# Optimization experiments

Hardware: AMD Instinct MI355X
Metric: run time of the kernel (lower is better)

## Reference

```python
import jax, jax.numpy as jnp
import numpy as np

B, S, D, H = 2, 4096, 768, 12
HD = D // H  # head_dim = 64


def setup_inputs() -> dict:
    key = jax.random.key(0)
    ks = jax.random.split(key, 12)
    s = 0.02
    inp = {
        'q': jax.random.normal(ks[0], (B, S, D), jnp.float32),
        'k': jax.random.normal(ks[1], (B, S, D), jnp.float32),
        'v': jax.random.normal(ks[2], (B, S, D), jnp.float32),
        # True = masked position (filled with -inf); causal mask, broadcastable
        'mask': jnp.triu(jnp.ones((S, S), jnp.bool_), k=1)[None, None],
        'Wq': jax.random.normal(ks[3], (D, D), jnp.float32) * s,
        'bq': jnp.zeros((D,), jnp.float32),
        'Wk': jax.random.normal(ks[4], (D, D), jnp.float32) * s,
        'bk': jnp.zeros((D,), jnp.float32),
        'Wv': jax.random.normal(ks[5], (D, D), jnp.float32) * s,
        'bv': jnp.zeros((D,), jnp.float32),
        'Wo': jax.random.normal(ks[6], (D, D), jnp.float32) * s,
        'bo': jnp.zeros((D,), jnp.float32),
    }
    return inp


def _split_heads(x):
    # [B, S, D] -> [B, H, S, HD]
    return x.reshape(B, S, H, HD).transpose(0, 2, 1, 3)


def reference(q, k, v, mask, Wq, bq, Wk, bk, Wv, bv, Wo, bo):
    # per-head linear projections (torch Linear: x @ W.T + b)
    qh = _split_heads(q @ Wq.T + bq)
    kh = _split_heads(k @ Wk.T + bk)
    vh = _split_heads(v @ Wv.T + bv)
    scale = 1.0 / np.sqrt(HD).astype(np.float32)
    # naive full [B, H, S, S] attention scores (module materializes these)
    wei = jnp.einsum('bhqd,bhkd->bhqk', qh, kh) * scale
    wei = jnp.where(mask, -jnp.inf, wei)
    attn = jax.nn.softmax(wei, axis=-1)
    feats = jnp.einsum('bhqk,bhkd->bhqd', attn, vh)
    # concat heads: [B, H, S, HD] -> [B, S, D]
    out = feats.transpose(0, 2, 1, 3).reshape(B, S, D)
    return out @ Wo.T + bo
```

## Files before the change

kernel.cpp:

```cpp
#include <hip/hip_runtime.h>
#include <math.h>

#define B_  2
#define S_  4096
#define D_  768
#define H_  12
#define HD_ 64

using bf16x8  = __attribute__((ext_vector_type(8))) __bf16;
using f32x4   = __attribute__((ext_vector_type(4))) float;
using ushort8 = __attribute__((ext_vector_type(8))) unsigned short;
using uintv2  = __attribute__((ext_vector_type(2))) unsigned;
using uintv4  = __attribute__((ext_vector_type(4))) unsigned;

__device__ __forceinline__ unsigned short f2b(float f) {
    union { float f; unsigned u; } x; x.f = f;
    unsigned r = x.u + 0x7fffu + ((x.u >> 16) & 1u);
    return (unsigned short)(r >> 16);
}
__device__ __forceinline__ unsigned pk2(float x, float y) {
    unsigned ux = __builtin_bit_cast(unsigned, x) + 0x8000u;
    unsigned uy = __builtin_bit_cast(unsigned, y) + 0x8000u;
    return (uy & 0xFFFF0000u) | (ux >> 16);
}
__device__ __forceinline__ unsigned cvtpk(float lo, float hi) {
    unsigned r;
    asm("v_cvt_pk_bf16_f32 %0, %1, %2" : "=v"(r) : "v"(lo), "v"(hi));
    return r;
}
__device__ __forceinline__ uintv2 xpose_pair(unsigned x, unsigned y) {
    uintv2 s = __builtin_amdgcn_permlane32_swap(x, y, false, false);
    return __builtin_amdgcn_permlane16_swap(s[0], s[1], false, false);
}

__global__ __launch_bounds__(256)
void w_convert(const float* __restrict__ Wq, const float* __restrict__ Wk,
               const float* __restrict__ Wv, const float* __restrict__ Wo,
               unsigned short* __restrict__ Wb)
{
    const int z = blockIdx.y;
    const float* src = (z == 0) ? Wq : (z == 1) ? Wk : (z == 2) ? Wv : Wo;
    unsigned short* dst = Wb + (size_t)z * (D_ * D_);
    int idx = blockIdx.x * 256 + threadIdx.x;
    const float4 a = *(const float4*)(src + (size_t)idx * 8);
    const float4 b = *(const float4*)(src + (size_t)idx * 8 + 4);
    uint4 o;
    o.x = pk2(a.x, a.y); o.y = pk2(a.z, a.w);
    o.z = pk2(b.x, b.y); o.w = pk2(b.z, b.w);
    *(uint4*)(dst + (size_t)idx * 8) = o;
}

__global__ __launch_bounds__(256)
void qkv_gemm(const float* __restrict__ q, const float* __restrict__ k,
              const float* __restrict__ v,
              const unsigned short* __restrict__ Wb,
              const float* __restrict__ bq, const float* __restrict__ bk,
              const float* __restrict__ bv,
              unsigned short* __restrict__ Qp, unsigned short* __restrict__ Kp,
              unsigned short* __restrict__ Vrm)
{
    constexpr int BM = 128, BN = 128, BK = 32, LDP = 40, NK = D_ / BK;
    const int lin = blockIdx.x;
    const int xcd = lin & 7, s = lin >> 3;
    const int z  = s / 48, rr = s % 48;
    const int bn = rr >> 3;
    const int bm = xcd * 8 + (rr & 7);

    const float* A    = (z == 0) ? q  : (z == 1) ? k  : v;
    const unsigned short* W = Wb + (size_t)z * (D_ * D_);
    const float* bias = (z == 0) ? bq : (z == 1) ? bk : bv;
    unsigned short* C = (z == 0) ? Qp : (z == 1) ? Kp : Vrm;

    __shared__ __align__(16) unsigned short As[2][BM * LDP];
    __shared__ __align__(16) unsigned short Bs[2][BN * LDP];

    const int tid = threadIdx.x;
    const int w = tid >> 6, lane = tid & 63, lr = lane & 15, lg = lane >> 4;
    const int wm = (w >> 1) * 64, wn = (w & 1) * 64;

    const int arow = tid >> 3, ac4 = (tid & 7) * 4;
    const int brow = tid >> 2, bc8 = (tid & 3) * 8;
    const float* Abase = A + (size_t)(bm * BM + arow) * D_ + ac4;
    const unsigned short* Wbase = W + (size_t)(bn * BN + brow) * D_ + bc8;

    float4 ap[4]; ushort8 bp[2];

    for (int t = 0; t < 4; ++t) ap[t] = *(const float4*)(Abase + (size_t)t * 32 * D_);
    for (int t = 0; t < 2; ++t) bp[t] = *(const ushort8*)(Wbase + (size_t)t * 64 * D_);
    for (int t = 0; t < 4; ++t)
        *(uint2*)&As[0][(arow + t * 32) * LDP + ac4] =
            make_uint2(pk2(ap[t].x, ap[t].y), pk2(ap[t].z, ap[t].w));
    for (int t = 0; t < 2; ++t)
        *(ushort8*)&Bs[0][(brow + t * 64) * LDP + bc8] = bp[t];
    __syncthreads();

    f32x4 acc[4][4] = {};

    for (int it = 0; it < NK; ++it) {
        const int cur = it & 1;
        const int k2 = ((it + 1 < NK) ? it + 1 : it) * BK;
        for (int t = 0; t < 4; ++t) ap[t] = *(const float4*)(Abase + k2 + (size_t)t * 32 * D_);
        for (int t = 0; t < 2; ++t) bp[t] = *(const ushort8*)(Wbase + k2 + (size_t)t * 64 * D_);

        bf16x8 af[4], bfr[4];
        for (int i = 0; i < 4; ++i) af[i]  = *(const bf16x8*)&As[cur][(wm + i * 16 + lr) * LDP + lg * 8];
        for (int j = 0; j < 4; ++j) bfr[j] = *(const bf16x8*)&Bs[cur][(wn + j * 16 + lr) * LDP + lg * 8];
        for (int i = 0; i < 4; ++i)
            for (int j = 0; j < 4; ++j)
                acc[i][j] = __builtin_amdgcn_mfma_f32_16x16x32_bf16(af[i], bfr[j], acc[i][j], 0, 0, 0);

        const int nxt = cur ^ 1;
        for (int t = 0; t < 4; ++t)
            *(uint2*)&As[nxt][(arow + t * 32) * LDP + ac4] =
                make_uint2(pk2(ap[t].x, ap[t].y), pk2(ap[t].z, ap[t].w));
        for (int t = 0; t < 2; ++t)
            *(ushort8*)&Bs[nxt][(brow + t * 64) * LDP + bc8] = bp[t];
        __syncthreads();
    }

    const float qscale = 0.18033688011112042f;
    for (int i = 0; i < 4; ++i) {
        int row0 = bm * BM + wm + i * 16 + lg * 4;
        for (int j = 0; j < 4; ++j) {
            int col = bn * BN + wn + j * 16 + lr;
            float bv_ = bias[col];
            for (int r = 0; r < 4; ++r) {
                float val = acc[i][j][r] + bv_;
                if (z == 0) val *= qscale;
                C[(size_t)(row0 + r) * D_ + col] = f2b(val);
            }
        }
    }
}

__global__ __launch_bounds__(256)
void v_transpose(const unsigned short* __restrict__ Vrm,
                 unsigned short* __restrict__ Vt)
{
    __shared__ __align__(16) unsigned short T[64][72];
    const int st = blockIdx.x, bh = blockIdx.y;
    const int b = bh / H_, h = bh % H_;
    const int tid = threadIdx.x;

    for (int t = 0; t < 2; ++t) {
        int idx = tid + t * 256, s = idx >> 3, c8 = (idx & 7) * 8;
        *(ushort8*)&T[s][c8] =
            *(const ushort8*)(Vrm + ((size_t)(b * S_ + st * 64 + s)) * D_ + h * HD_ + c8);
    }
    __syncthreads();
    const int d = tid >> 2;
    for (int it = 0; it < 2; ++it) {
        int s8 = (tid & 3) + it * 4;
        ushort8 val;
        for (int j = 0; j < 8; ++j) val[j] = T[s8 * 8 + j][d];
        *(ushort8*)(Vt + ((size_t)bh * HD_ + d) * S_ + st * 64 + s8 * 8) = val;
    }
}

__global__ __launch_bounds__(256)
void o_gemm(const unsigned short* __restrict__ Ai, const unsigned short* __restrict__ W,
            const float* __restrict__ bias, float* __restrict__ C)
{
    constexpr int BM = 128, BN = 64, BK = 32, LDP = 40, NK = D_ / BK;
    __shared__ __align__(16) unsigned short As[2][BM * LDP];
    __shared__ __align__(16) unsigned short Bs[2][BN * LDP];

    const int lin = blockIdx.x;
    const int xcd = lin & 7, s = lin >> 3;
    const int bn = s >> 3;
    const int bm = xcd * 8 + (s & 7);

    const int tid = threadIdx.x;
    const int w = tid >> 6, lane = tid & 63, lr = lane & 15, lg = lane >> 4;
    const int wm = (w >> 1) * 64, wn = (w & 1) * 32;

    const int arow = tid >> 2, ac8 = (tid & 3) * 8;
    const unsigned short* Abase = Ai + (size_t)(bm * BM + arow) * D_ + ac8;
    const unsigned short* Wbase = W + (size_t)(bn * BN + arow) * D_ + ac8;

    ushort8 apre[2], bpre;
    for (int t = 0; t < 2; ++t) apre[t] = *(const ushort8*)(Abase + (size_t)t * 64 * D_);
    bpre = *(const ushort8*)(Wbase);
    for (int t = 0; t < 2; ++t)
        *(ushort8*)&As[0][(arow + t * 64) * LDP + ac8] = apre[t];
    *(ushort8*)&Bs[0][arow * LDP + ac8] = bpre;
    __syncthreads();

    f32x4 acc[4][2] = {};

    for (int it = 0; it < NK; ++it) {
        const int cur = it & 1;
        const int k2 = ((it + 1 < NK) ? it + 1 : it) * BK;
        for (int t = 0; t < 2; ++t) apre[t] = *(const ushort8*)(Abase + k2 + (size_t)t * 64 * D_);
        bpre = *(const ushort8*)(Wbase + k2);

        bf16x8 af[4], bfr[2];
        for (int i = 0; i < 4; ++i) af[i]  = *(const bf16x8*)&As[cur][(wm + i * 16 + lr) * LDP + lg * 8];
        for (int j = 0; j < 2; ++j) bfr[j] = *(const bf16x8*)&Bs[cur][(wn + j * 16 + lr) * LDP + lg * 8];
        for (int i = 0; i < 4; ++i)
            for (int j = 0; j < 2; ++j)
                acc[i][j] = __builtin_amdgcn_mfma_f32_16x16x32_bf16(af[i], bfr[j], acc[i][j], 0, 0, 0);

        const int nxt = cur ^ 1;
        for (int t = 0; t < 2; ++t)
            *(ushort8*)&As[nxt][(arow + t * 64) * LDP + ac8] = apre[t];
        *(ushort8*)&Bs[nxt][arow * LDP + ac8] = bpre;
        __syncthreads();
    }

    for (int i = 0; i < 4; ++i) {
        int row0 = bm * BM + wm + i * 16 + lg * 4;
        for (int j = 0; j < 2; ++j) {
            int col = bn * BN + wn + j * 16 + lr;
            float bv_ = bias[col];
            for (int r = 0; r < 4; ++r)
                C[(size_t)(row0 + r) * D_ + col] = acc[i][j][r] + bv_;
        }
    }
}

__global__ __launch_bounds__(256)
void attn_kernel(const unsigned short* __restrict__ Qp,
                 const unsigned short* __restrict__ Kp,
                 const unsigned short* __restrict__ Vt,
                 unsigned short* __restrict__ feats)
{
    __shared__ __align__(16) unsigned short Ks[2][64 * 72];
    __shared__ __align__(16) unsigned short Vs[2][64 * 72];

    const int tid = threadIdx.x;
    const int lin = blockIdx.x + gridDim.x * blockIdx.y;
    const int xcd = lin & 7, idx = lin >> 3;
    const int bhl = idx >> 5;
    const int i   = idx & 31;
    int p;
    if (bhl == 0)      p = i;
    else if (bhl == 1) p = (i + 16) & 31;
    else               p = (i < 16) ? (31 - 2 * i) : (62 - 2 * i);
    const int bh  = xcd * 3 + bhl;
    const int b = bh / H_, h = bh % H_;
    const int w = tid >> 6, lane = tid & 63, lr = lane & 15, lg = lane >> 4;

    const int qtA = 63 - p, qtB = p;

    bf16x8 ones;
    for (int j = 0; j < 8; ++j) ones[j] = (__bf16)1.0f;

    const size_t kbase = ((size_t)b * S_) * D_ + h * HD_;
    const size_t vbase = ((size_t)bh * HD_) * S_;

    const size_t qbA = ((size_t)(b * S_ + qtA * 64 + w * 16 + lr)) * D_ + h * HD_;
    const size_t qbB = ((size_t)(b * S_ + qtB * 64 + w * 16 + lr)) * D_ + h * HD_;
    bf16x8 qfA0 = *(const bf16x8*)(Qp + qbA + lg * 8);
    bf16x8 qfA1 = *(const bf16x8*)(Qp + qbA + 32 + lg * 8);
    bf16x8 qfB0 = *(const bf16x8*)(Qp + qbB + lg * 8);
    bf16x8 qfB1 = *(const bf16x8*)(Qp + qbB + 32 + lg * 8);

    f32x4 oA[4] = {}, oB[4] = {};
    f32x4 lA = {0.f, 0.f, 0.f, 0.f}, lB = {0.f, 0.f, 0.f, 0.f};

    const int nst = qtA + 1;

    const int srow = tid >> 3, sc8 = (tid & 7) * 8;
    const unsigned short* kpt = Kp + kbase + (size_t)srow * D_ + sc8;
    const unsigned short* vpt = Vt + vbase + (size_t)srow * S_ + sc8;
    unsigned short* KsW0 = &Ks[0][srow * 72 + sc8];
    unsigned short* VsW0 = &Vs[0][srow * 72 + sc8];
    unsigned short* KsW1 = &Ks[1][srow * 72 + sc8];
    unsigned short* VsW1 = &Vs[1][srow * 72 + sc8];

    {
        ushort8 a0 = *(const ushort8*)(kpt);
        ushort8 a1 = *(const ushort8*)(kpt + (size_t)32 * D_);
        ushort8 a2 = *(const ushort8*)(vpt);
        ushort8 a3 = *(const ushort8*)(vpt + (size_t)32 * S_);
        *(ushort8*)KsW0            = a0;
        *(ushort8*)(KsW0 + 32*72)  = a1;
        *(ushort8*)VsW0            = a2;
        *(ushort8*)(VsW0 + 32*72)  = a3;
    }
    __syncthreads();

    for (int kb = 0; kb < nst; ++kb) {
        const bool bAct = (kb <= qtB);
        const int cur = kb & 1;
        const unsigned short* Kc = Ks[cur];
        const unsigned short* Vc = Vs[cur];

        const int kb2 = (kb + 1 < nst) ? kb + 1 : kb;
        const unsigned short* kp2 = kpt + (size_t)kb2 * 64 * D_;
        const unsigned short* vp2 = vpt + (size_t)kb2 * 64;
        ushort8 kr0 = *(const ushort8*)(kp2);
        ushort8 kr1 = *(const ushort8*)(kp2 + (size_t)32 * D_);
        ushort8 vr0 = *(const ushort8*)(vp2);
        ushort8 vr1 = *(const ushort8*)(vp2 + (size_t)32 * S_);

        bf16x8 kf[4][2];
        for (int n = 0; n < 4; ++n) {
            kf[n][0] = *(const bf16x8*)&Kc[(n * 16 + lr) * 72 + lg * 8];
            kf[n][1] = *(const bf16x8*)&Kc[(n * 16 + lr) * 72 + 32 + lg * 8];
        }

        bf16x8 pfA0, pfA1, pfB0, pfB1;

        {
            f32x4 st[4];
            for (int n = 0; n < 4; ++n) {
                f32x4 s = {0.f, 0.f, 0.f, 0.f};
                s = __builtin_amdgcn_mfma_f32_16x16x32_bf16(kf[n][0], qfA0, s, 0, 0, 0);
                s = __builtin_amdgcn_mfma_f32_16x16x32_bf16(kf[n][1], qfA1, s, 0, 0, 0);
                st[n] = s;
            }
            if (kb == qtA) {
                for (int n = 0; n < 4; ++n)
                    for (int r = 0; r < 4; ++r)
                        if (n * 16 + lg * 4 + r > w * 16 + lr) st[n][r] = -INFINITY;
            }
            unsigned a_[4][2];
            for (int n = 0; n < 4; ++n) {
                float e0 = __builtin_amdgcn_exp2f(st[n][0]);
                float e1 = __builtin_amdgcn_exp2f(st[n][1]);
                float e2 = __builtin_amdgcn_exp2f(st[n][2]);
                float e3 = __builtin_amdgcn_exp2f(st[n][3]);
                a_[n][0] = cvtpk(e0, e1);
                a_[n][1] = cvtpk(e2, e3);
            }
            uintv2 p00 = xpose_pair(a_[0][0], a_[1][0]);
            uintv2 p01 = xpose_pair(a_[0][1], a_[1][1]);
            uintv2 p10 = xpose_pair(a_[2][0], a_[3][0]);
            uintv2 p11 = xpose_pair(a_[2][1], a_[3][1]);
            uintv4 w0 = {p00[0], p01[0], p00[1], p01[1]};
            uintv4 w1 = {p10[0], p11[0], p10[1], p11[1]};
            pfA0 = __builtin_bit_cast(bf16x8, w0);
            pfA1 = __builtin_bit_cast(bf16x8, w1);
        }
        if (bAct) {
            f32x4 st[4];
            for (int n = 0; n < 4; ++n) {
                f32x4 s = {0.f, 0.f, 0.f, 0.f};
                s = __builtin_amdgcn_mfma_f32_16x16x32_bf16(kf[n][0], qfB0, s, 0, 0, 0);
                s = __builtin_amdgcn_mfma_f32_16x16x32_bf16(kf[n][1], qfB1, s, 0, 0, 0);
                st[n] = s;
            }
            if (kb == qtB) {
                for (int n = 0; n < 4; ++n)
                    for (int r = 0; r < 4; ++r)
                        if (n * 16 + lg * 4 + r > w * 16 + lr) st[n][r] = -INFINITY;
            }
            unsigned a_[4][2];
            for (int n = 0; n < 4; ++n) {
                float e0 = __builtin_amdgcn_exp2f(st[n][0]);
                float e1 = __builtin_amdgcn_exp2f(st[n][1]);
                float e2 = __builtin_amdgcn_exp2f(st[n][2]);
                float e3 = __builtin_amdgcn_exp2f(st[n][3]);
                a_[n][0] = cvtpk(e0, e1);
                a_[n][1] = cvtpk(e2, e3);
            }
            uintv2 p00 = xpose_pair(a_[0][0], a_[1][0]);
            uintv2 p01 = xpose_pair(a_[0][1], a_[1][1]);
            uintv2 p10 = xpose_pair(a_[2][0], a_[3][0]);
            uintv2 p11 = xpose_pair(a_[2][1], a_[3][1]);
            uintv4 w0 = {p00[0], p01[0], p00[1], p01[1]};
            uintv4 w1 = {p10[0], p11[0], p10[1], p11[1]};
            pfB0 = __builtin_bit_cast(bf16x8, w0);
            pfB1 = __builtin_bit_cast(bf16x8, w1);
        }

        bf16x8 vf[4][2];
        for (int n = 0; n < 4; ++n) {
            vf[n][0] = *(const bf16x8*)&Vc[(n * 16 + lr) * 72 + lg * 8];
            vf[n][1] = *(const bf16x8*)&Vc[(n * 16 + lr) * 72 + 32 + lg * 8];
        }
        {
            for (int n = 0; n < 4; ++n) {
                oA[n] = __builtin_amdgcn_mfma_f32_16x16x32_bf16(vf[n][0], pfA0, oA[n], 0, 0, 0);
                oA[n] = __builtin_amdgcn_mfma_f32_16x16x32_bf16(vf[n][1], pfA1, oA[n], 0, 0, 0);
            }
            lA = __builtin_amdgcn_mfma_f32_16x16x32_bf16(ones, pfA0, lA, 0, 0, 0);
            lA = __builtin_amdgcn_mfma_f32_16x16x32_bf16(ones, pfA1, lA, 0, 0, 0);
        }
        if (bAct) {
            for (int n = 0; n < 4; ++n) {
                oB[n] = __builtin_amdgcn_mfma_f32_16x16x32_bf16(vf[n][0], pfB0, oB[n], 0, 0, 0);
                oB[n] = __builtin_amdgcn_mfma_f32_16x16x32_bf16(vf[n][1], pfB1, oB[n], 0, 0, 0);
            }
            lB = __builtin_amdgcn_mfma_f32_16x16x32_bf16(ones, pfB0, lB, 0, 0, 0);
            lB = __builtin_amdgcn_mfma_f32_16x16x32_bf16(ones, pfB1, lB, 0, 0, 0);
        }

        if (cur == 0) {
            *(ushort8*)KsW1            = kr0;
            *(ushort8*)(KsW1 + 32*72)  = kr1;
            *(ushort8*)VsW1            = vr0;
            *(ushort8*)(VsW1 + 32*72)  = vr1;
        } else {
            *(ushort8*)KsW0            = kr0;
            *(ushort8*)(KsW0 + 32*72)  = kr1;
            *(ushort8*)VsW0            = vr0;
            *(ushort8*)(VsW0 + 32*72)  = vr1;
        }
        __syncthreads();
    }

    {
        const float inv = 1.0f / lA[0];
        const size_t obase = ((size_t)(b * S_ + qtA * 64 + w * 16 + lr)) * D_ + h * HD_;
        for (int n = 0; n < 4; ++n) {
            unsigned short e0 = f2b(oA[n][0] * inv), e1 = f2b(oA[n][1] * inv);
            unsigned short e2 = f2b(oA[n][2] * inv), e3 = f2b(oA[n][3] * inv);
            *(uint2*)(feats + obase + n * 16 + lg * 4) =
                make_uint2((unsigned)e0 | ((unsigned)e1 << 16),
                           (unsigned)e2 | ((unsigned)e3 << 16));
        }
    }
    {
        const float inv = 1.0f / lB[0];
        const size_t obase = ((size_t)(b * S_ + qtB * 64 + w * 16 + lr)) * D_ + h * HD_;
        for (int n = 0; n < 4; ++n) {
            unsigned short e0 = f2b(oB[n][0] * inv), e1 = f2b(oB[n][1] * inv);
            unsigned short e2 = f2b(oB[n][2] * inv), e3 = f2b(oB[n][3] * inv);
            *(uint2*)(feats + obase + n * 16 + lg * 4) =
                make_uint2((unsigned)e0 | ((unsigned)e1 << 16),
                           (unsigned)e2 | ((unsigned)e3 << 16));
        }
    }
}

extern "C" void kernel_launch(void* const* d_in, const int* in_sizes, int n_in,
                              void* d_out, int out_size, void* d_ws, size_t ws_size,
                              hipStream_t stream) {
    const float* q  = (const float*)d_in[0];
    const float* k  = (const float*)d_in[1];
    const float* v  = (const float*)d_in[2];
    const float* Wq = (const float*)d_in[4];
    const float* bq = (const float*)d_in[5];
    const float* Wk = (const float*)d_in[6];
    const float* bk = (const float*)d_in[7];
    const float* Wv = (const float*)d_in[8];
    const float* bv = (const float*)d_in[9];
    const float* Wo = (const float*)d_in[10];
    const float* bo = (const float*)d_in[11];
    float* out = (float*)d_out;

    const size_t npro = (size_t)B_ * S_ * D_;
    const size_t nw   = (size_t)D_ * D_;
    unsigned short* Qp    = (unsigned short*)d_ws;
    unsigned short* Kp    = Qp + npro;
    unsigned short* Vrm   = Kp + npro;
    unsigned short* Vt    = Vrm + npro;
    unsigned short* Wb    = Vt + npro;
    unsigned short* feats = Vrm;

    dim3 blk(256);
    w_convert<<<dim3(288, 4), blk, 0, stream>>>(Wq, Wk, Wv, Wo, Wb);
    qkv_gemm<<<dim3(1152), blk, 0, stream>>>(q, k, v, Wb, bq, bk, bv,
                                             Qp, Kp, Vrm);
    v_transpose<<<dim3(S_ / 64, B_ * H_), blk, 0, stream>>>(Vrm, Vt);
    attn_kernel<<<dim3(32, B_ * H_), blk, 0, stream>>>(Qp, Kp, Vt, feats);
    o_gemm<<<dim3(768), blk, 0, stream>>>(feats, Wb + 3 * nw, bo, out);
}
```

Measured before the change: 327.3 us.

## Fuse V transpose into QKV GEMM epilogue and raise MFMA wave priority

The QKV projection epilogue now writes V directly in the head-major transposed layout the attention kernel consumes, so the separate v_transpose kernel and its intermediate buffer go away. This saves one launch plus a full read and write of V. The transposed stores are 8-byte scattered writes and less coalesced than before. Separately, the attention kernel raises wave priority around its MFMA blocks to help the scheduler overlap matrix work with other waves.

```diff
diff --git a/kernel.cpp b/kernel.cpp
--- a/kernel.cpp
+++ b/kernel.cpp
@@ -57,7 +57,7 @@
               const float* __restrict__ bq, const float* __restrict__ bk,
               const float* __restrict__ bv,
               unsigned short* __restrict__ Qp, unsigned short* __restrict__ Kp,
-              unsigned short* __restrict__ Vrm)
+              unsigned short* __restrict__ Vt)
 {
     constexpr int BM = 128, BN = 128, BK = 32, LDP = 40, NK = D_ / BK;
     const int lin = blockIdx.x;
@@ -69,7 +69,6 @@
     const float* A    = (z == 0) ? q  : (z == 1) ? k  : v;
     const unsigned short* W = Wb + (size_t)z * (D_ * D_);
     const float* bias = (z == 0) ? bq : (z == 1) ? bk : bv;
-    unsigned short* C = (z == 0) ? Qp : (z == 1) ? Kp : Vrm;
 
     __shared__ __align__(16) unsigned short As[2][BM * LDP];
     __shared__ __align__(16) unsigned short Bs[2][BN * LDP];
@@ -118,42 +117,38 @@
         __syncthreads();
     }
 
-    const float qscale = 0.18033688011112042f;
-    for (int i = 0; i < 4; ++i) {
-        int row0 = bm * BM + wm + i * 16 + lg * 4;
+    if (z == 2) {
         for (int j = 0; j < 4; ++j) {
-            int col = bn * BN + wn + j * 16 + lr;
-            float bv_ = bias[col];
-            for (int r = 0; r < 4; ++r) {
-                float val = acc[i][j][r] + bv_;
-                if (z == 0) val *= qscale;
-                C[(size_t)(row0 + r) * D_ + col] = f2b(val);
-            }
-        }
-    }
-}
-
-__global__ __launch_bounds__(256)
-void v_transpose(const unsigned short* __restrict__ Vrm,
-                 unsigned short* __restrict__ Vt)
-{
-    __shared__ __align__(16) unsigned short T[64][72];
-    const int st = blockIdx.x, bh = blockIdx.y;
-    const int b = bh / H_, h = bh % H_;
-    const int tid = threadIdx.x;
-
-    for (int t = 0; t < 2; ++t) {
-        int idx = tid + t * 256, s = idx >> 3, c8 = (idx & 7) * 8;
-        *(ushort8*)&T[s][c8] =
-            *(const ushort8*)(Vrm + ((size_t)(b * S_ + st * 64 + s)) * D_ + h * HD_ + c8);
-    }
-    __syncthreads();
-    const int d = tid >> 2;
-    for (int it = 0; it < 2; ++it) {
-        int s8 = (tid & 3) + it * 4;
-        ushort8 val;
-        for (int j = 0; j < 8; ++j) val[j] = T[s8 * 8 + j][d];
-        *(ushort8*)(Vt + ((size_t)bh * HD_ + d) * S_ + st * 64 + s8 * 8) = val;
+            const int col = bn * BN + wn + j * 16 + lr;
+            const int hh = col >> 6, dd = col & 63;
+            const float bv_ = bias[col];
+            for (int i = 0; i < 4; ++i) {
+                const int s_g = bm * BM + wm + i * 16 + lg * 4;
+                const int bb = s_g >> 12, s_in = s_g & 4095;
+                unsigned short e0 = f2b(acc[i][j][0] + bv_);
+                unsigned short e1 = f2b(acc[i][j][1] + bv_);
+                unsigned short e2 = f2b(acc[i][j][2] + bv_);
+                unsigned short e3 = f2b(acc[i][j][3] + bv_);
+                *(uint2*)(Vt + ((size_t)((bb * H_ + hh) * HD_ + dd)) * S_ + s_in) =
+                    make_uint2((unsigned)e0 | ((unsigned)e1 << 16),
+                               (unsigned)e2 | ((unsigned)e3 << 16));
+            }
+        }
+    } else {
+        unsigned short* C = (z == 0) ? Qp : Kp;
+        const float qscale = 0.18033688011112042f;
+        for (int i = 0; i < 4; ++i) {
+            int row0 = bm * BM + wm + i * 16 + lg * 4;
+            for (int j = 0; j < 4; ++j) {
+                int col = bn * BN + wn + j * 16 + lr;
+                float bv_ = bias[col];
+                for (int r = 0; r < 4; ++r) {
+                    float val = acc[i][j][r] + bv_;
+                    if (z == 0) val *= qscale;
+                    C[(size_t)(row0 + r) * D_ + col] = f2b(val);
+                }
+            }
+        }
     }
 }
 
@@ -305,12 +300,14 @@
 
         {
             f32x4 st[4];
+            __builtin_amdgcn_s_setprio(1);
             for (int n = 0; n < 4; ++n) {
                 f32x4 s = {0.f, 0.f, 0.f, 0.f};
                 s = __builtin_amdgcn_mfma_f32_16x16x32_bf16(kf[n][0], qfA0, s, 0, 0, 0);
                 s = __builtin_amdgcn_mfma_f32_16x16x32_bf16(kf[n][1], qfA1, s, 0, 0, 0);
                 st[n] = s;
             }
+            __builtin_amdgcn_s_setprio(0);
             if (kb == qtA) {
                 for (int n = 0; n < 4; ++n)
                     for (int r = 0; r < 4; ++r)
@@ -336,12 +333,14 @@
         }
         if (bAct) {
             f32x4 st[4];
+            __builtin_amdgcn_s_setprio(1);
             for (int n = 0; n < 4; ++n) {
                 f32x4 s = {0.f, 0.f, 0.f, 0.f};
                 s = __builtin_amdgcn_mfma_f32_16x16x32_bf16(kf[n][0], qfB0, s, 0, 0, 0);
                 s = __builtin_amdgcn_mfma_f32_16x16x32_bf16(kf[n][1], qfB1, s, 0, 0, 0);
                 st[n] = s;
             }
+            __builtin_amdgcn_s_setprio(0);
             if (kb == qtB) {
                 for (int n = 0; n < 4; ++n)
                     for (int r = 0; r < 4; ++r)
@@ -372,20 +371,24 @@
             vf[n][1] = *(const bf16x8*)&Vc[(n * 16 + lr) * 72 + 32 + lg * 8];
         }
         {
+            __builtin_amdgcn_s_setprio(1);
             for (int n = 0; n < 4; ++n) {
                 oA[n] = __builtin_amdgcn_mfma_f32_16x16x32_bf16(vf[n][0], pfA0, oA[n], 0, 0, 0);
                 oA[n] = __builtin_amdgcn_mfma_f32_16x16x32_bf16(vf[n][1], pfA1, oA[n], 0, 0, 0);
             }
             lA = __builtin_amdgcn_mfma_f32_16x16x32_bf16(ones, pfA0, lA, 0, 0, 0);
             lA = __builtin_amdgcn_mfma_f32_16x16x32_bf16(ones, pfA1, lA, 0, 0, 0);
+            __builtin_amdgcn_s_setprio(0);
         }
         if (bAct) {
+            __builtin_amdgcn_s_setprio(1);
             for (int n = 0; n < 4; ++n) {
                 oB[n] = __builtin_amdgcn_mfma_f32_16x16x32_bf16(vf[n][0], pfB0, oB[n], 0, 0, 0);
                 oB[n] = __builtin_amdgcn_mfma_f32_16x16x32_bf16(vf[n][1], pfB1, oB[n], 0, 0, 0);
             }
             lB = __builtin_amdgcn_mfma_f32_16x16x32_bf16(ones, pfB0, lB, 0, 0, 0);
             lB = __builtin_amdgcn_mfma_f32_16x16x32_bf16(ones, pfB1, lB, 0, 0, 0);
+            __builtin_amdgcn_s_setprio(0);
         }
 
         if (cur == 0) {
@@ -446,16 +449,14 @@
     const size_t nw   = (size_t)D_ * D_;
     unsigned short* Qp    = (unsigned short*)d_ws;
     unsigned short* Kp    = Qp + npro;
-    unsigned short* Vrm   = Kp + npro;
-    unsigned short* Vt    = Vrm + npro;
+    unsigned short* feats = Kp + npro;
+    unsigned short* Vt    = feats + npro;
     unsigned short* Wb    = Vt + npro;
-    unsigned short* feats = Vrm;
 
     dim3 blk(256);
     w_convert<<<dim3(288, 4), blk, 0, stream>>>(Wq, Wk, Wv, Wo, Wb);
     qkv_gemm<<<dim3(1152), blk, 0, stream>>>(q, k, v, Wb, bq, bk, bv,
-                                             Qp, Kp, Vrm);
-    v_transpose<<<dim3(S_ / 64, B_ * H_), blk, 0, stream>>>(Vrm, Vt);
+                                             Qp, Kp, Vt);
     attn_kernel<<<dim3(32, B_ * H_), blk, 0, stream>>>(Qp, Kp, Vt, feats);
     o_gemm<<<dim3(768), blk, 0, stream>>>(feats, Wb + 3 * nw, bo, out);
 }
```

Result: slower. 348.5 us (+6.5%).
